# Performance work log

Measured on AMD Instinct MI355X. Metric: run time of the kernel, lower is better.

The kernel has to match this reference:

```python
import jax, jax.numpy as jnp
import numpy as np

N_NODES = 100000   # nodes per node type
N_EDGES = 800000   # edges per edge type
F_IN = 128         # lazy (-1,-1) input feature dim, chosen == hidden
HID = 128          # hidden_channels
OUT = 1            # out_channels
N_LAYERS = 2
B = 256            # batch_size (num graphs)
NEG_SLOPE = 0.2    # GATConv default leaky_relu slope


def setup_inputs() -> dict:
    key = jax.random.key(0)
    ks = jax.random.split(key, 16)
    x_i = jax.random.normal(ks[0], (N_NODES, F_IN), jnp.float32)
    x_j = jax.random.normal(ks[1], (N_NODES, F_IN), jnp.float32)
    ei_ii = jax.random.randint(ks[2], (2, N_EDGES), 0, N_NODES, jnp.int32)
    ei_jj = jax.random.randint(ks[3], (2, N_EDGES), 0, N_NODES, jnp.int32)
    ei_ij = jax.random.randint(ks[4], (2, N_EDGES), 0, N_NODES, jnp.int32)
    ei_ji = jax.random.randint(ks[5], (2, N_EDGES), 0, N_NODES, jnp.int32)
    batch_i = jnp.sort(jax.random.randint(ks[6], (N_NODES,), 0, B, jnp.int32))
    batch_j = jnp.sort(jax.random.randint(ks[7], (N_NODES,), 0, B, jnp.int32))
    s = 1.0 / np.sqrt(HID)
    Ws = jax.random.normal(ks[8], (N_LAYERS, 4, F_IN, HID), jnp.float32) * s
    Wd = jax.random.normal(ks[9], (N_LAYERS, 4, F_IN, HID), jnp.float32) * s
    att_s = jax.random.normal(ks[10], (N_LAYERS, 4, HID), jnp.float32) * s
    att_d = jax.random.normal(ks[11], (N_LAYERS, 4, HID), jnp.float32) * s
    bias = jnp.zeros((N_LAYERS, 4, HID), jnp.float32)
    lin_w = jax.random.normal(ks[12], (HID, OUT), jnp.float32) * s
    lin_b = jnp.zeros((OUT,), jnp.float32)
    return dict(x_i=x_i, x_j=x_j, ei_ii=ei_ii, ei_jj=ei_jj, ei_ij=ei_ij,
                ei_ji=ei_ji, batch_i=batch_i, batch_j=batch_j, Ws=Ws, Wd=Wd,
                att_s=att_s, att_d=att_d, bias=bias, lin_w=lin_w, lin_b=lin_b)


def gat_conv(x_src, x_dst, edge, W_s, W_d, a_s, a_d, b):
    """Single-head GATConv: gather -> edge attention -> segment softmax -> scatter."""
    src, dst = edge[0], edge[1]
    n_dst = x_dst.shape[0]
    hs = x_src @ W_s                      # [Ns, C]
    hd = x_dst @ W_d                      # [Nd, C]
    e = jax.nn.leaky_relu((hs * a_s).sum(-1)[src] + (hd * a_d).sum(-1)[dst],
                          NEG_SLOPE)      # [E]
    m = jax.ops.segment_max(e, dst, num_segments=n_dst)
    m = jnp.where(jnp.isfinite(m), m, 0.0)  # empty segments -> 0
    p = jnp.exp(e - m[dst])
    denom = jax.ops.segment_sum(p, dst, num_segments=n_dst)
    alpha = p / jnp.maximum(denom[dst], 1e-16)
    out = jax.ops.segment_sum(alpha[:, None] * hs[src], dst, num_segments=n_dst)
    return out + b


def mean_pool(x, batch, size):
    s = jax.ops.segment_sum(x, batch, num_segments=size)
    cnt = jax.ops.segment_sum(jnp.ones((x.shape[0],), x.dtype), batch,
                              num_segments=size)
    return s / jnp.maximum(cnt, 1.0)[:, None]


def reference(x_i, x_j, ei_ii, ei_jj, ei_ij, ei_ji, batch_i, batch_j,
              Ws, Wd, att_s, att_d, bias, lin_w, lin_b):
    xi, xj = x_i, x_j
    for l in range(N_LAYERS):
        # edge-type order: 0=inner_i, 1=inner_j, 2=outer_ij, 3=outer_ji
        out_i = (gat_conv(xi, xi, ei_ii, Ws[l, 0], Wd[l, 0], att_s[l, 0], att_d[l, 0], bias[l, 0])
                 + gat_conv(xj, xi, ei_ji, Ws[l, 3], Wd[l, 3], att_s[l, 3], att_d[l, 3], bias[l, 3]))
        out_j = (gat_conv(xj, xj, ei_jj, Ws[l, 1], Wd[l, 1], att_s[l, 1], att_d[l, 1], bias[l, 1])
                 + gat_conv(xi, xj, ei_ij, Ws[l, 2], Wd[l, 2], att_s[l, 2], att_d[l, 2], bias[l, 2]))
        xi, xj = jnp.tanh(out_i), jnp.tanh(out_j)
    p_i = mean_pool(xi, batch_i, B)       # [B, HID]
    p_j = mean_pool(xj, batch_j, B)       # [B, HID]
    x = 0.5 * (p_i + p_j)                 # mean over the stacked pair
    return jax.nn.sigmoid(x @ lin_w + lin_b)
```

## Files before the change

kernel.cpp:

```cpp
#include <hip/hip_runtime.h>


#define NEG_SLOPE 0.2f

typedef __attribute__((ext_vector_type(8))) short short8v;
typedef __attribute__((ext_vector_type(4))) float float4v;

__device__ __forceinline__ unsigned short f2bf(float f) {
  unsigned u = __float_as_uint(f);
  unsigned r = (u + 0x7FFFu + ((u >> 16) & 1u)) >> 16;
  return (unsigned short)r;
}
__device__ __forceinline__ unsigned pack2(float a, float b) {
  return (unsigned)f2bf(a) | ((unsigned)f2bf(b) << 16);
}
__device__ __forceinline__ float bflo(unsigned u) {
  return __uint_as_float(u << 16);
}
__device__ __forceinline__ float bfhi(unsigned u) {
  return __uint_as_float(u & 0xFFFF0000u);
}
__device__ __forceinline__ float rl_f(float x, int lane) {
  return __int_as_float(__builtin_amdgcn_readlane(__float_as_int(x), lane));
}
__device__ __forceinline__ int rl_i(int x, int lane) {
  return __builtin_amdgcn_readlane(x, lane);
}

__global__ __launch_bounds__(256) void w_to_bf16t(const float* __restrict__ W,
                                                  unsigned short* __restrict__ Wt) {
  __shared__ float buf[64][129];
  int b = blockIdx.x, t = threadIdx.x;
  const float* w = W + (size_t)b * 16384;
  unsigned short* o = Wt + (size_t)b * 16384;
  for (int h = 0; h < 2; ++h) {
    for (int i = 0; i < 32; ++i) {
      int idx = i * 256 + t;
      buf[idx >> 7][idx & 127] = w[(size_t)(h * 64 + (idx >> 7)) * 128 + (idx & 127)];
    }
    __syncthreads();
    for (int i = 0; i < 32; ++i) {
      int idx = i * 256 + t;
      o[(size_t)(idx >> 6) * 128 + h * 64 + (idx & 63)] = f2bf(buf[idx & 63][idx >> 6]);
    }
    __syncthreads();
  }
}

__global__ void precompute_wa(const float* __restrict__ W,
                              const float* __restrict__ att,
                              float* __restrict__ out) {
  int idx = blockIdx.x;
  int f = threadIdx.x;
  const float* w = W + (size_t)idx * 128 * 128 + (size_t)f * 128;
  const float* a = att + idx * 128;
  float s = 0.f;
  #pragma unroll 8
  for (int h = 0; h < 128; ++h) s += w[h] * a[h];
  out[idx * 128 + f] = s;
}

template <int XBF16>
__global__ __launch_bounds__(256) void gemm_dual(
    const void* __restrict__ Xv,
    const unsigned short* __restrict__ Wt1, const float* __restrict__ att1,
    unsigned short* __restrict__ Hb1, float* __restrict__ as1,
    const unsigned short* __restrict__ Wt2, const float* __restrict__ att2,
    unsigned short* __restrict__ Hb2, float* __restrict__ as2,
    const float* __restrict__ vdA, const float* __restrict__ vdB,
    float* __restrict__ adA, float* __restrict__ adB, int M) {
  __shared__ unsigned short Xt[64][136];
  __shared__ unsigned short Wt[128][136];
  const int t = threadIdx.x;
  const int row0 = blockIdx.x * 64;

  {
    int r = t >> 2;
    int cq = (t & 3) * 32;
    int gr = row0 + r;
    if (gr >= M) gr = M - 1;
    if (XBF16) {
      const unsigned short* Xb = (const unsigned short*)Xv;
      const uint4* src = (const uint4*)(Xb + (size_t)gr * 128 + cq);
      #pragma unroll
      for (int i = 0; i < 4; ++i) *(uint4*)&Xt[r][cq + i * 8] = src[i];
    } else {
      const float* Xf = (const float*)Xv;
      const float4* src = (const float4*)(Xf + (size_t)gr * 128 + cq);
      #pragma unroll
      for (int i = 0; i < 8; ++i) {
        float4 v = src[i];
        uint2 u;
        u.x = pack2(v.x, v.y);
        u.y = pack2(v.z, v.w);
        *(uint2*)&Xt[r][cq + i * 4] = u;
      }
    }
  }
  {
    int n = t >> 1;
    int kh = (t & 1) * 64;
    const uint4* src = (const uint4*)(Wt1 + (size_t)n * 128 + kh);
    #pragma unroll
    for (int i = 0; i < 8; ++i) *(uint4*)&Wt[n][kh + i * 8] = src[i];
  }
  __syncthreads();

  if (t < 128) {
    int r = t & 63;
    const float* vd = (t < 64) ? vdA : vdB;
    float* adout = (t < 64) ? adA : adB;
    float sum = 0.f;
    #pragma unroll 4
    for (int k8 = 0; k8 < 16; ++k8) {
      uint4 u = *(const uint4*)&Xt[r][k8 * 8];
      const float* v = vd + k8 * 8;
      sum = fmaf(bflo(u.x), v[0], sum);
      sum = fmaf(bfhi(u.x), v[1], sum);
      sum = fmaf(bflo(u.y), v[2], sum);
      sum = fmaf(bfhi(u.y), v[3], sum);
      sum = fmaf(bflo(u.z), v[4], sum);
      sum = fmaf(bfhi(u.z), v[5], sum);
      sum = fmaf(bflo(u.w), v[6], sum);
      sum = fmaf(bfhi(u.w), v[7], sum);
    }
    int gr = row0 + r;
    if (gr < M) adout[gr] = sum;
  }

  const int lane = t & 63;
  const int wv = t >> 6;
  const int m = lane & 15;
  const int g = lane >> 4;
  const int ws = wv * 16;

  for (int ww = 0; ww < 2; ++ww) {
    if (ww == 1) {
      __syncthreads();
      int n = t >> 1;
      int kh = (t & 1) * 64;
      const uint4* src = (const uint4*)(Wt2 + (size_t)n * 128 + kh);
      #pragma unroll
      for (int i = 0; i < 8; ++i) *(uint4*)&Wt[n][kh + i * 8] = src[i];
      __syncthreads();
    }
    const float* att = ww ? att2 : att1;
    unsigned short* Hb = ww ? Hb2 : Hb1;
    float* as_ = ww ? as2 : as1;

    float4v acc[8];
    float4v z = {0.f, 0.f, 0.f, 0.f};
    #pragma unroll
    for (int nt = 0; nt < 8; ++nt) acc[nt] = z;

    #pragma unroll
    for (int ks = 0; ks < 4; ++ks) {
      short8v a = *(const short8v*)&Xt[ws + m][ks * 32 + g * 8];
      #pragma unroll
      for (int nt = 0; nt < 8; ++nt) {
        short8v b = *(const short8v*)&Wt[nt * 16 + m][ks * 32 + g * 8];
        acc[nt] = __builtin_amdgcn_mfma_f32_16x16x32_bf16(a, b, acc[nt], 0, 0, 0);
      }
    }

    {
      float attv[8];
      #pragma unroll
      for (int nt = 0; nt < 8; ++nt) attv[nt] = att[nt * 16 + m];
      #pragma unroll
      for (int r = 0; r < 4; ++r) {
        float s = 0.f;
        #pragma unroll
        for (int nt = 0; nt < 8; ++nt) s = fmaf(acc[nt][r], attv[nt], s);
        #pragma unroll
        for (int off = 1; off < 16; off <<= 1) s += __shfl_xor(s, off);
        if (m == 0) {
          int grow = row0 + ws + g * 4 + r;
          if (grow < M) as_[grow] = s;
        }
      }
    }

    #pragma unroll
    for (int nt = 0; nt < 8; ++nt) {
      #pragma unroll
      for (int r = 0; r < 4; ++r) {
        float v = acc[nt][r];
        float vn = __shfl_xor(v, 1);
        if ((m & 1) == 0) {
          int grow = row0 + ws + g * 4 + r;
          if (grow < M) {
            *(unsigned*)(Hb + (size_t)grow * 128 + nt * 16 + m) = pack2(v, vn);
          }
        }
      }
    }
  }
}

__global__ void hist4(const int* __restrict__ e0, const int* __restrict__ e1,
                      const int* __restrict__ e2, const int* __restrict__ e3,
                      int E, int* __restrict__ deg, int N) {
  int i = blockIdx.x * 256 + threadIdx.x;
  if (i >= E) return;
  int t = blockIdx.y;
  const int* ei = (t == 0) ? e0 : (t == 1) ? e1 : (t == 2) ? e2 : e3;
  atomicAdd(&deg[t * N + ei[E + i]], 1);
}

__global__ __launch_bounds__(1024) void scan4(const int* __restrict__ deg,
                                              int* __restrict__ rowptr, int N) {
  __shared__ int sums[1024];
  int t = threadIdx.x;
  int ty = blockIdx.x;
  const int* d = deg + (size_t)ty * N;
  int* rp = rowptr + (size_t)ty * (N + 1);
  int chunk = (N + 1023) / 1024;
  int lo = t * chunk;
  int hi = lo + chunk; if (hi > N) hi = N; if (lo > N) lo = N;
  int s = 0;
  for (int i = lo; i < hi; ++i) s += d[i];
  sums[t] = s;
  __syncthreads();
  for (int off = 1; off < 1024; off <<= 1) {
    int add = (t >= off) ? sums[t - off] : 0;
    __syncthreads();
    sums[t] += add;
    __syncthreads();
  }
  int run = (t == 0) ? 0 : sums[t - 1];
  for (int i = lo; i < hi; ++i) {
    rp[i] = run;
    run += d[i];
  }
  if (t == 1023) rp[N] = sums[1023];
}

__global__ void fill4(const int* __restrict__ e0, const int* __restrict__ e1,
                      const int* __restrict__ e2, const int* __restrict__ e3,
                      int E, const int* __restrict__ rowptr,
                      int* __restrict__ fill, int* __restrict__ csrc, int N) {
  int i = blockIdx.x * 256 + threadIdx.x;
  if (i >= E) return;
  int t = blockIdx.y;
  const int* ei = (t == 0) ? e0 : (t == 1) ? e1 : (t == 2) ? e2 : e3;
  int d = ei[E + i];
  int s = ei[i];
  int pos = rowptr[(size_t)t * (N + 1) + d] + atomicAdd(&fill[t * N + d], 1);
  csrc[(size_t)t * E + pos] = s;
}

struct PairArgs {
  const int* rA; const int* sA; const unsigned short* hA;
  const float* asA; const float* adA;
  const int* rB; const int* sB; const unsigned short* hB;
  const float* asB; const float* adB;
  const float* biasA; const float* biasB;
};

__device__ __forceinline__ void agg_pair(const PairArgs& P, int n, int lane,
                                         float2& outA, float2& outB) {
  int begA = P.rA[n], endA = P.rA[n + 1];
  int begB = P.rB[n], endB = P.rB[n + 1];
  float adA = P.adA[n], adB = P.adB[n];
  float lsA = 0.f, lsB = 0.f;
  float2 aA = make_float2(0.f, 0.f), aB = make_float2(0.f, 0.f);
  int cA = begA, cB = begB;
  while (cA < endA || cB < endB) {
    int kA = cA + lane, kB = cB + lane;
    bool vA = kA < endA;
    bool vB = kB < endB;
    int sA = vA ? P.sA[kA] : 0;
    int sB = vB ? P.sB[kB] : 0;
    float eA = vA ? (P.asA[sA] + adA) : 0.f;
    float eB = vB ? (P.asB[sB] + adB) : 0.f;
    eA = eA > 0.f ? eA : NEG_SLOPE * eA;
    eB = eB > 0.f ? eB : NEG_SLOPE * eB;
    float pA = vA ? __expf(eA) : 0.f;
    float pB = vB ? __expf(eB) : 0.f;
    int cntA = endA - cA; cntA = cntA < 0 ? 0 : (cntA > 64 ? 64 : cntA);
    int cntB = endB - cB; cntB = cntB < 0 ? 0 : (cntB > 64 ? 64 : cntB);
    int cnt = cntA > cntB ? cntA : cntB;
    for (int base = 0; base < cnt; base += 8) {
      float qa0 = rl_f(pA, base + 0), qa1 = rl_f(pA, base + 1);
      float qa2 = rl_f(pA, base + 2), qa3 = rl_f(pA, base + 3);
      float qa4 = rl_f(pA, base + 4), qa5 = rl_f(pA, base + 5);
      float qa6 = rl_f(pA, base + 6), qa7 = rl_f(pA, base + 7);
      float qb0 = rl_f(pB, base + 0), qb1 = rl_f(pB, base + 1);
      float qb2 = rl_f(pB, base + 2), qb3 = rl_f(pB, base + 3);
      float qb4 = rl_f(pB, base + 4), qb5 = rl_f(pB, base + 5);
      float qb6 = rl_f(pB, base + 6), qb7 = rl_f(pB, base + 7);
      int ta0 = rl_i(sA, base + 0), ta1 = rl_i(sA, base + 1);
      int ta2 = rl_i(sA, base + 2), ta3 = rl_i(sA, base + 3);
      int ta4 = rl_i(sA, base + 4), ta5 = rl_i(sA, base + 5);
      int ta6 = rl_i(sA, base + 6), ta7 = rl_i(sA, base + 7);
      int tb0 = rl_i(sB, base + 0), tb1 = rl_i(sB, base + 1);
      int tb2 = rl_i(sB, base + 2), tb3 = rl_i(sB, base + 3);
      int tb4 = rl_i(sB, base + 4), tb5 = rl_i(sB, base + 5);
      int tb6 = rl_i(sB, base + 6), tb7 = rl_i(sB, base + 7);
      unsigned ua0 = *(const unsigned*)(P.hA + (size_t)ta0 * 128 + lane * 2);
      unsigned ua1 = *(const unsigned*)(P.hA + (size_t)ta1 * 128 + lane * 2);
      unsigned ua2 = *(const unsigned*)(P.hA + (size_t)ta2 * 128 + lane * 2);
      unsigned ua3 = *(const unsigned*)(P.hA + (size_t)ta3 * 128 + lane * 2);
      unsigned ua4 = *(const unsigned*)(P.hA + (size_t)ta4 * 128 + lane * 2);
      unsigned ua5 = *(const unsigned*)(P.hA + (size_t)ta5 * 128 + lane * 2);
      unsigned ua6 = *(const unsigned*)(P.hA + (size_t)ta6 * 128 + lane * 2);
      unsigned ua7 = *(const unsigned*)(P.hA + (size_t)ta7 * 128 + lane * 2);
      unsigned ub0 = *(const unsigned*)(P.hB + (size_t)tb0 * 128 + lane * 2);
      unsigned ub1 = *(const unsigned*)(P.hB + (size_t)tb1 * 128 + lane * 2);
      unsigned ub2 = *(const unsigned*)(P.hB + (size_t)tb2 * 128 + lane * 2);
      unsigned ub3 = *(const unsigned*)(P.hB + (size_t)tb3 * 128 + lane * 2);
      unsigned ub4 = *(const unsigned*)(P.hB + (size_t)tb4 * 128 + lane * 2);
      unsigned ub5 = *(const unsigned*)(P.hB + (size_t)tb5 * 128 + lane * 2);
      unsigned ub6 = *(const unsigned*)(P.hB + (size_t)tb6 * 128 + lane * 2);
      unsigned ub7 = *(const unsigned*)(P.hB + (size_t)tb7 * 128 + lane * 2);
      lsA += ((qa0 + qa1) + (qa2 + qa3)) + ((qa4 + qa5) + (qa6 + qa7));
      lsB += ((qb0 + qb1) + (qb2 + qb3)) + ((qb4 + qb5) + (qb6 + qb7));
      aA.x = fmaf(qa0, bflo(ua0), aA.x); aA.y = fmaf(qa0, bfhi(ua0), aA.y);
      aA.x = fmaf(qa1, bflo(ua1), aA.x); aA.y = fmaf(qa1, bfhi(ua1), aA.y);
      aA.x = fmaf(qa2, bflo(ua2), aA.x); aA.y = fmaf(qa2, bfhi(ua2), aA.y);
      aA.x = fmaf(qa3, bflo(ua3), aA.x); aA.y = fmaf(qa3, bfhi(ua3), aA.y);
      aA.x = fmaf(qa4, bflo(ua4), aA.x); aA.y = fmaf(qa4, bfhi(ua4), aA.y);
      aA.x = fmaf(qa5, bflo(ua5), aA.x); aA.y = fmaf(qa5, bfhi(ua5), aA.y);
      aA.x = fmaf(qa6, bflo(ua6), aA.x); aA.y = fmaf(qa6, bfhi(ua6), aA.y);
      aA.x = fmaf(qa7, bflo(ua7), aA.x); aA.y = fmaf(qa7, bfhi(ua7), aA.y);
      aB.x = fmaf(qb0, bflo(ub0), aB.x); aB.y = fmaf(qb0, bfhi(ub0), aB.y);
      aB.x = fmaf(qb1, bflo(ub1), aB.x); aB.y = fmaf(qb1, bfhi(ub1), aB.y);
      aB.x = fmaf(qb2, bflo(ub2), aB.x); aB.y = fmaf(qb2, bfhi(ub2), aB.y);
      aB.x = fmaf(qb3, bflo(ub3), aB.x); aB.y = fmaf(qb3, bfhi(ub3), aB.y);
      aB.x = fmaf(qb4, bflo(ub4), aB.x); aB.y = fmaf(qb4, bfhi(ub4), aB.y);
      aB.x = fmaf(qb5, bflo(ub5), aB.x); aB.y = fmaf(qb5, bfhi(ub5), aB.y);
      aB.x = fmaf(qb6, bflo(ub6), aB.x); aB.y = fmaf(qb6, bfhi(ub6), aB.y);
      aB.x = fmaf(qb7, bflo(ub7), aB.x); aB.y = fmaf(qb7, bfhi(ub7), aB.y);
    }
    cA += 64;
    cB += 64;
  }
  float invA = 1.f / fmaxf(lsA, 1e-16f);
  float invB = 1.f / fmaxf(lsB, 1e-16f);
  outA = make_float2(aA.x * invA, aA.y * invA);
  outB = make_float2(aB.x * invB, aB.y * invB);
}

__global__ __launch_bounds__(256) void agg_store2(
    PairArgs P0, unsigned short* __restrict__ out0,
    PairArgs P1, unsigned short* __restrict__ out1, int N) {
  int wave = (blockIdx.x * 256 + threadIdx.x) >> 6;
  int lane = threadIdx.x & 63;
  if (wave >= N) return;
  const PairArgs& P = blockIdx.y ? P1 : P0;
  unsigned short* out = blockIdx.y ? out1 : out0;
  float2 a, b;
  agg_pair(P, wave, lane, a, b);
  float2 b1 = *(const float2*)(P.biasA + lane * 2);
  float2 b2 = *(const float2*)(P.biasB + lane * 2);
  float vx = tanhf(a.x + b.x + b1.x + b2.x);
  float vy = tanhf(a.y + b.y + b1.y + b2.y);
  *(unsigned*)(out + (size_t)wave * 128 + lane * 2) = pack2(vx, vy);
}

__global__ __launch_bounds__(256) void agg_pool2(
    PairArgs P0, const int* __restrict__ batch0, float* __restrict__ pool0,
    PairArgs P1, const int* __restrict__ batch1, float* __restrict__ pool1,
    int N) {
  int wave = (blockIdx.x * 256 + threadIdx.x) >> 6;
  int lane = threadIdx.x & 63;
  if (wave >= N) return;
  const PairArgs& P = blockIdx.y ? P1 : P0;
  const int* batch = blockIdx.y ? batch1 : batch0;
  float* pool = blockIdx.y ? pool1 : pool0;
  float2 a, b;
  agg_pair(P, wave, lane, a, b);
  float2 b1 = *(const float2*)(P.biasA + lane * 2);
  float2 b2 = *(const float2*)(P.biasB + lane * 2);
  float vx = tanhf(a.x + b.x + b1.x + b2.x);
  float vy = tanhf(a.y + b.y + b1.y + b2.y);
  int bb = batch[wave];
  float* p = pool + (size_t)bb * 128 + lane * 2;
  unsafeAtomicAdd(p, vx);
  unsafeAtomicAdd(p + 1, vy);
}

__device__ __forceinline__ int lower_bound_i(const int* __restrict__ a, int n,
                                             int v) {
  int lo = 0, hi = n;
  while (lo < hi) {
    int mid = (lo + hi) >> 1;
    if (a[mid] < v) lo = mid + 1; else hi = mid;
  }
  return lo;
}

__global__ void final_k(const float* __restrict__ pool_i,
                        const int* __restrict__ batch_i,
                        const float* __restrict__ pool_j,
                        const int* __restrict__ batch_j, int N,
                        const float* __restrict__ lin_w,
                        const float* __restrict__ lin_b,
                        float* __restrict__ out) {
  int b = threadIdx.x;
  float ci = (float)(lower_bound_i(batch_i, N, b + 1) -
                     lower_bound_i(batch_i, N, b));
  float cj = (float)(lower_bound_i(batch_j, N, b + 1) -
                     lower_bound_i(batch_j, N, b));
  ci = fmaxf(ci, 1.f);
  cj = fmaxf(cj, 1.f);
  float acc = 0.f;
  #pragma unroll 4
  for (int f = 0; f < 128; ++f) {
    float x = 0.5f * (pool_i[(size_t)b * 128 + f] / ci +
                      pool_j[(size_t)b * 128 + f] / cj);
    acc += x * lin_w[f];
  }
  acc += lin_b[0];
  out[b] = 1.f / (1.f + __expf(-acc));
}

extern "C" void kernel_launch(void* const* d_in, const int* in_sizes, int n_in,
                              void* d_out, int out_size, void* d_ws,
                              size_t ws_size, hipStream_t stream) {
  const float* x_i = (const float*)d_in[0];
  const float* x_j = (const float*)d_in[1];
  const int* ei_arr[4] = {(const int*)d_in[2], (const int*)d_in[3],
                          (const int*)d_in[4], (const int*)d_in[5]};
  const int* batch_i = (const int*)d_in[6];
  const int* batch_j = (const int*)d_in[7];
  const float* Ws = (const float*)d_in[8];
  const float* Wd = (const float*)d_in[9];
  const float* att_s = (const float*)d_in[10];
  const float* att_d = (const float*)d_in[11];
  const float* bias = (const float*)d_in[12];
  const float* lin_w = (const float*)d_in[13];
  const float* lin_b = (const float*)d_in[14];
  float* out = (float*)d_out;

  const int N = in_sizes[0] / 128;
  const int E = in_sizes[2] / 2;
  const size_t NF = (size_t)N * 128;

  char* w = (char*)d_ws;
  auto alloc = [&](size_t bytes) {
    char* p = w;
    w += (bytes + 255) & ~(size_t)255;
    return p;
  };
  unsigned short* bufA_i = (unsigned short*)alloc(NF * 2);
  unsigned short* bufA_j = (unsigned short*)alloc(NF * 2);
  unsigned short* hsb[4];
  for (int c = 0; c < 4; ++c) hsb[c] = (unsigned short*)alloc(NF * 2);
  int* csrc = (int*)alloc((size_t)4 * E * 4);
  int* rowptr = (int*)alloc((size_t)4 * (N + 1) * 4);
  int* deg = (int*)alloc((size_t)4 * N * 4);
  int* fillc = (int*)alloc((size_t)4 * N * 4);
  float* asb[4];
  for (int c = 0; c < 4; ++c) asb[c] = (float*)alloc((size_t)N * 4);
  float* adb[4];
  for (int c = 0; c < 4; ++c) adb[c] = (float*)alloc((size_t)N * 4);
  float* wdad = (float*)alloc(8 * 128 * 4);
  unsigned short* Wst = (unsigned short*)alloc(8 * 16384 * 2);
  float* pool = (float*)alloc(2 * 256 * 128 * 4);
  float* pool_i = pool;
  float* pool_j = pool + 256 * 128;

  w_to_bf16t<<<8, 256, 0, stream>>>(Ws, Wst);
  precompute_wa<<<8, 128, 0, stream>>>(Wd, att_d, wdad);

  hipMemsetAsync(deg, 0, (size_t)4 * N * 4, stream);
  hipMemsetAsync(fillc, 0, (size_t)4 * N * 4, stream);
  dim3 egrid((E + 255) / 256, 4);
  hist4<<<egrid, 256, 0, stream>>>(ei_arr[0], ei_arr[1], ei_arr[2], ei_arr[3],
                                   E, deg, N);
  scan4<<<4, 1024, 0, stream>>>(deg, rowptr, N);
  fill4<<<egrid, 256, 0, stream>>>(ei_arr[0], ei_arr[1], ei_arr[2], ei_arr[3],
                                   E, rowptr, fillc, csrc, N);

  hipMemsetAsync(pool, 0, 2 * 256 * 128 * 4, stream);

  const int gemm_blocks = (N + 63) / 64;
  const int nodew_blocks = (N + 3) / 4;

  for (int l = 0; l < 2; ++l) {
    const void* cur_i = (l == 0) ? (const void*)x_i : (const void*)bufA_i;
    const void* cur_j = (l == 0) ? (const void*)x_j : (const void*)bufA_j;
    const size_t L = (size_t)l * 4;

    if (l == 0) {
      gemm_dual<0><<<gemm_blocks, 256, 0, stream>>>(
          cur_i, Wst + (L + 0) * 16384, att_s + (L + 0) * 128, hsb[0], asb[0],
          Wst + (L + 2) * 16384, att_s + (L + 2) * 128, hsb[2], asb[2],
          wdad + (L + 0) * 128, wdad + (L + 3) * 128, adb[0], adb[3], N);
      gemm_dual<0><<<gemm_blocks, 256, 0, stream>>>(
          cur_j, Wst + (L + 1) * 16384, att_s + (L + 1) * 128, hsb[1], asb[1],
          Wst + (L + 3) * 16384, att_s + (L + 3) * 128, hsb[3], asb[3],
          wdad + (L + 1) * 128, wdad + (L + 2) * 128, adb[1], adb[2], N);
    } else {
      gemm_dual<1><<<gemm_blocks, 256, 0, stream>>>(
          cur_i, Wst + (L + 0) * 16384, att_s + (L + 0) * 128, hsb[0], asb[0],
          Wst + (L + 2) * 16384, att_s + (L + 2) * 128, hsb[2], asb[2],
          wdad + (L + 0) * 128, wdad + (L + 3) * 128, adb[0], adb[3], N);
      gemm_dual<1><<<gemm_blocks, 256, 0, stream>>>(
          cur_j, Wst + (L + 1) * 16384, att_s + (L + 1) * 128, hsb[1], asb[1],
          Wst + (L + 3) * 16384, att_s + (L + 3) * 128, hsb[3], asb[3],
          wdad + (L + 1) * 128, wdad + (L + 2) * 128, adb[1], adb[2], N);
    }

    PairArgs P0 = {rowptr + (size_t)0 * (N + 1), csrc + (size_t)0 * E, hsb[0],
                   asb[0], adb[0],
                   rowptr + (size_t)3 * (N + 1), csrc + (size_t)3 * E, hsb[3],
                   asb[3], adb[3],
                   bias + (L + 0) * 128, bias + (L + 3) * 128};
    PairArgs P1 = {rowptr + (size_t)1 * (N + 1), csrc + (size_t)1 * E, hsb[1],
                   asb[1], adb[1],
                   rowptr + (size_t)2 * (N + 1), csrc + (size_t)2 * E, hsb[2],
                   asb[2], adb[2],
                   bias + (L + 1) * 128, bias + (L + 2) * 128};

    dim3 agrid(nodew_blocks, 2);
    if (l == 0) {
      agg_store2<<<agrid, 256, 0, stream>>>(P0, bufA_i, P1, bufA_j, N);
    } else {
      agg_pool2<<<agrid, 256, 0, stream>>>(P0, batch_i, pool_i, P1, batch_j,
                                           pool_j, N);
    }
  }

  final_k<<<1, 256, 0, stream>>>(pool_i, batch_i, pool_j, batch_j, N, lin_w,
                                 lin_b, out);
}
```

Baseline: 1.109 ms.

## Store projected features as fp8, merge dual GEMM launches, grid-stride edge kernels

The per-edge-type projected source features are now stored as packed fp8 instead of bf16 and unpacked with the hardware fp8-to-f32 conversion in the aggregation gather, halving the bytes fetched per gathered neighbour row. The two per-layer GEMM launches are merged into one 2D grid that picks its inputs from blockIdx.y. The histogram and CSR-fill kernels switch to a fixed 512-block grid-stride loop. fp8 storage adds noticeable quantization error to the messages and may break accuracy tolerance.

Result: faster. 1.036 ms, median of 2 (-6.6%).

```diff
diff --git a/kernel.cpp b/kernel.cpp
--- a/kernel.cpp
+++ b/kernel.cpp
@@ -5,6 +5,7 @@
 
 typedef __attribute__((ext_vector_type(8))) short short8v;
 typedef __attribute__((ext_vector_type(4))) float float4v;
+typedef __attribute__((ext_vector_type(2))) float float2v;
 
 __device__ __forceinline__ unsigned short f2bf(float f) {
   unsigned u = __float_as_uint(f);
@@ -60,19 +61,25 @@
   out[idx * 128 + f] = s;
 }
 
+struct GemmArgs {
+  const unsigned short* Wt1; const float* att1;
+  unsigned char* Hb1; float* as1;
+  const unsigned short* Wt2; const float* att2;
+  unsigned char* Hb2; float* as2;
+  const float* vdA; const float* vdB;
+  float* adA; float* adB;
+};
+
 template <int XBF16>
-__global__ __launch_bounds__(256) void gemm_dual(
-    const void* __restrict__ Xv,
-    const unsigned short* __restrict__ Wt1, const float* __restrict__ att1,
-    unsigned short* __restrict__ Hb1, float* __restrict__ as1,
-    const unsigned short* __restrict__ Wt2, const float* __restrict__ att2,
-    unsigned short* __restrict__ Hb2, float* __restrict__ as2,
-    const float* __restrict__ vdA, const float* __restrict__ vdB,
-    float* __restrict__ adA, float* __restrict__ adB, int M) {
+__global__ __launch_bounds__(256) void gemm_dual2(
+    const void* __restrict__ X0, const void* __restrict__ X1,
+    GemmArgs Ga, GemmArgs Gb, int M) {
   __shared__ unsigned short Xt[64][136];
   __shared__ unsigned short Wt[128][136];
   const int t = threadIdx.x;
   const int row0 = blockIdx.x * 64;
+  const void* Xv = blockIdx.y ? X1 : X0;
+  const GemmArgs& G = blockIdx.y ? Gb : Ga;
 
   {
     int r = t >> 2;
@@ -100,7 +107,7 @@
   {
     int n = t >> 1;
     int kh = (t & 1) * 64;
-    const uint4* src = (const uint4*)(Wt1 + (size_t)n * 128 + kh);
+    const uint4* src = (const uint4*)(G.Wt1 + (size_t)n * 128 + kh);
     #pragma unroll
     for (int i = 0; i < 8; ++i) *(uint4*)&Wt[n][kh + i * 8] = src[i];
   }
@@ -108,8 +115,8 @@
 
   if (t < 128) {
     int r = t & 63;
-    const float* vd = (t < 64) ? vdA : vdB;
-    float* adout = (t < 64) ? adA : adB;
+    const float* vd = (t < 64) ? G.vdA : G.vdB;
+    float* adout = (t < 64) ? G.adA : G.adB;
     float sum = 0.f;
     #pragma unroll 4
     for (int k8 = 0; k8 < 16; ++k8) {
@@ -139,14 +146,14 @@
       __syncthreads();
       int n = t >> 1;
       int kh = (t & 1) * 64;
-      const uint4* src = (const uint4*)(Wt2 + (size_t)n * 128 + kh);
+      const uint4* src = (const uint4*)(G.Wt2 + (size_t)n * 128 + kh);
       #pragma unroll
       for (int i = 0; i < 8; ++i) *(uint4*)&Wt[n][kh + i * 8] = src[i];
       __syncthreads();
     }
-    const float* att = ww ? att2 : att1;
-    unsigned short* Hb = ww ? Hb2 : Hb1;
-    float* as_ = ww ? as2 : as1;
+    const float* att = ww ? G.att2 : G.att1;
+    unsigned char* Hb = ww ? G.Hb2 : G.Hb1;
+    float* as_ = ww ? G.as2 : G.as1;
 
     float4v acc[8];
     float4v z = {0.f, 0.f, 0.f, 0.f};
@@ -190,7 +197,9 @@
         if ((m & 1) == 0) {
           int grow = row0 + ws + g * 4 + r;
           if (grow < M) {
-            *(unsigned*)(Hb + (size_t)grow * 128 + nt * 16 + m) = pack2(v, vn);
+            int pk = __builtin_amdgcn_cvt_pk_fp8_f32(v, vn, 0, false);
+            *(unsigned short*)(Hb + (size_t)grow * 128 + nt * 16 + m) =
+                (unsigned short)(pk & 0xFFFF);
           }
         }
       }
@@ -201,11 +210,11 @@
 __global__ void hist4(const int* __restrict__ e0, const int* __restrict__ e1,
                       const int* __restrict__ e2, const int* __restrict__ e3,
                       int E, int* __restrict__ deg, int N) {
-  int i = blockIdx.x * 256 + threadIdx.x;
-  if (i >= E) return;
   int t = blockIdx.y;
   const int* ei = (t == 0) ? e0 : (t == 1) ? e1 : (t == 2) ? e2 : e3;
-  atomicAdd(&deg[t * N + ei[E + i]], 1);
+  int stride = gridDim.x * 256;
+  for (int i = blockIdx.x * 256 + threadIdx.x; i < E; i += stride)
+    atomicAdd(&deg[t * N + ei[E + i]], 1);
 }
 
 __global__ __launch_bounds__(1024) void scan4(const int* __restrict__ deg,
@@ -240,23 +249,28 @@
                       const int* __restrict__ e2, const int* __restrict__ e3,
                       int E, const int* __restrict__ rowptr,
                       int* __restrict__ fill, int* __restrict__ csrc, int N) {
-  int i = blockIdx.x * 256 + threadIdx.x;
-  if (i >= E) return;
   int t = blockIdx.y;
   const int* ei = (t == 0) ? e0 : (t == 1) ? e1 : (t == 2) ? e2 : e3;
-  int d = ei[E + i];
-  int s = ei[i];
-  int pos = rowptr[(size_t)t * (N + 1) + d] + atomicAdd(&fill[t * N + d], 1);
-  csrc[(size_t)t * E + pos] = s;
+  int stride = gridDim.x * 256;
+  for (int i = blockIdx.x * 256 + threadIdx.x; i < E; i += stride) {
+    int d = ei[E + i];
+    int s = ei[i];
+    int pos = rowptr[(size_t)t * (N + 1) + d] + atomicAdd(&fill[t * N + d], 1);
+    csrc[(size_t)t * E + pos] = s;
+  }
 }
 
 struct PairArgs {
-  const int* rA; const int* sA; const unsigned short* hA;
+  const int* rA; const int* sA; const unsigned char* hA;
   const float* asA; const float* adA;
-  const int* rB; const int* sB; const unsigned short* hB;
+  const int* rB; const int* sB; const unsigned char* hB;
   const float* asB; const float* adB;
   const float* biasA; const float* biasB;
 };
+
+#define GATH(P_h, idx, dst) {                                           \
+  unsigned short uu = *(const unsigned short*)((P_h) + (size_t)(idx) * 128 + lane * 2); \
+  dst = __builtin_amdgcn_cvt_pk_f32_fp8((int)uu, false); }
 
 __device__ __forceinline__ void agg_pair(const PairArgs& P, int n, int lane,
                                          float2& outA, float2& outB) {
@@ -298,40 +312,34 @@
       int tb2 = rl_i(sB, base + 2), tb3 = rl_i(sB, base + 3);
       int tb4 = rl_i(sB, base + 4), tb5 = rl_i(sB, base + 5);
       int tb6 = rl_i(sB, base + 6), tb7 = rl_i(sB, base + 7);
-      unsigned ua0 = *(const unsigned*)(P.hA + (size_t)ta0 * 128 + lane * 2);
-      unsigned ua1 = *(const unsigned*)(P.hA + (size_t)ta1 * 128 + lane * 2);
-      unsigned ua2 = *(const unsigned*)(P.hA + (size_t)ta2 * 128 + lane * 2);
-      unsigned ua3 = *(const unsigned*)(P.hA + (size_t)ta3 * 128 + lane * 2);
-      unsigned ua4 = *(const unsigned*)(P.hA + (size_t)ta4 * 128 + lane * 2);
-      unsigned ua5 = *(const unsigned*)(P.hA + (size_t)ta5 * 128 + lane * 2);
-      unsigned ua6 = *(const unsigned*)(P.hA + (size_t)ta6 * 128 + lane * 2);
-      unsigned ua7 = *(const unsigned*)(P.hA + (size_t)ta7 * 128 + lane * 2);
-      unsigned ub0 = *(const unsigned*)(P.hB + (size_t)tb0 * 128 + lane * 2);
-      unsigned ub1 = *(const unsigned*)(P.hB + (size_t)tb1 * 128 + lane * 2);
-      unsigned ub2 = *(const unsigned*)(P.hB + (size_t)tb2 * 128 + lane * 2);
-      unsigned ub3 = *(const unsigned*)(P.hB + (size_t)tb3 * 128 + lane * 2);
-      unsigned ub4 = *(const unsigned*)(P.hB + (size_t)tb4 * 128 + lane * 2);
-      unsigned ub5 = *(const unsigned*)(P.hB + (size_t)tb5 * 128 + lane * 2);
-      unsigned ub6 = *(const unsigned*)(P.hB + (size_t)tb6 * 128 + lane * 2);
-      unsigned ub7 = *(const unsigned*)(P.hB + (size_t)tb7 * 128 + lane * 2);
+      float2v ha0, ha1, ha2, ha3, ha4, ha5, ha6, ha7;
+      float2v hb0, hb1, hb2, hb3, hb4, hb5, hb6, hb7;
+      GATH(P.hA, ta0, ha0) GATH(P.hA, ta1, ha1)
+      GATH(P.hA, ta2, ha2) GATH(P.hA, ta3, ha3)
+      GATH(P.hA, ta4, ha4) GATH(P.hA, ta5, ha5)
+      GATH(P.hA, ta6, ha6) GATH(P.hA, ta7, ha7)
+      GATH(P.hB, tb0, hb0) GATH(P.hB, tb1, hb1)
+      GATH(P.hB, tb2, hb2) GATH(P.hB, tb3, hb3)
+      GATH(P.hB, tb4, hb4) GATH(P.hB, tb5, hb5)
+      GATH(P.hB, tb6, hb6) GATH(P.hB, tb7, hb7)
       lsA += ((qa0 + qa1) + (qa2 + qa3)) + ((qa4 + qa5) + (qa6 + qa7));
       lsB += ((qb0 + qb1) + (qb2 + qb3)) + ((qb4 + qb5) + (qb6 + qb7));
-      aA.x = fmaf(qa0, bflo(ua0), aA.x); aA.y = fmaf(qa0, bfhi(ua0), aA.y);
-      aA.x = fmaf(qa1, bflo(ua1), aA.x); aA.y = fmaf(qa1, bfhi(ua1), aA.y);
-      aA.x = fmaf(qa2, bflo(ua2), aA.x); aA.y = fmaf(qa2, bfhi(ua2), aA.y);
-      aA.x = fmaf(qa3, bflo(ua3), aA.x); aA.y = fmaf(qa3, bfhi(ua3), aA.y);
-      aA.x = fmaf(qa4, bflo(ua4), aA.x); aA.y = fmaf(qa4, bfhi(ua4), aA.y);
-      aA.x = fmaf(qa5, bflo(ua5), aA.x); aA.y = fmaf(qa5, bfhi(ua5), aA.y);
-      aA.x = fmaf(qa6, bflo(ua6), aA.x); aA.y = fmaf(qa6, bfhi(ua6), aA.y);
-      aA.x = fmaf(qa7, bflo(ua7), aA.x); aA.y = fmaf(qa7, bfhi(ua7), aA.y);
-      aB.x = fmaf(qb0, bflo(ub0), aB.x); aB.y = fmaf(qb0, bfhi(ub0), aB.y);
-      aB.x = fmaf(qb1, bflo(ub1), aB.x); aB.y = fmaf(qb1, bfhi(ub1), aB.y);
-      aB.x = fmaf(qb2, bflo(ub2), aB.x); aB.y = fmaf(qb2, bfhi(ub2), aB.y);
-      aB.x = fmaf(qb3, bflo(ub3), aB.x); aB.y = fmaf(qb3, bfhi(ub3), aB.y);
-      aB.x = fmaf(qb4, bflo(ub4), aB.x); aB.y = fmaf(qb4, bfhi(ub4), aB.y);
-      aB.x = fmaf(qb5, bflo(ub5), aB.x); aB.y = fmaf(qb5, bfhi(ub5), aB.y);
-      aB.x = fmaf(qb6, bflo(ub6), aB.x); aB.y = fmaf(qb6, bfhi(ub6), aB.y);
-      aB.x = fmaf(qb7, bflo(ub7), aB.x); aB.y = fmaf(qb7, bfhi(ub7), aB.y);
+      aA.x = fmaf(qa0, ha0[0], aA.x); aA.y = fmaf(qa0, ha0[1], aA.y);
+      aA.x = fmaf(qa1, ha1[0], aA.x); aA.y = fmaf(qa1, ha1[1], aA.y);
+      aA.x = fmaf(qa2, ha2[0], aA.x); aA.y = fmaf(qa2, ha2[1], aA.y);
+      aA.x = fmaf(qa3, ha3[0], aA.x); aA.y = fmaf(qa3, ha3[1], aA.y);
+      aA.x = fmaf(qa4, ha4[0], aA.x); aA.y = fmaf(qa4, ha4[1], aA.y);
+      aA.x = fmaf(qa5, ha5[0], aA.x); aA.y = fmaf(qa5, ha5[1], aA.y);
+      aA.x = fmaf(qa6, ha6[0], aA.x); aA.y = fmaf(qa6, ha6[1], aA.y);
+      aA.x = fmaf(qa7, ha7[0], aA.x); aA.y = fmaf(qa7, ha7[1], aA.y);
+      aB.x = fmaf(qb0, hb0[0], aB.x); aB.y = fmaf(qb0, hb0[1], aB.y);
+      aB.x = fmaf(qb1, hb1[0], aB.x); aB.y = fmaf(qb1, hb1[1], aB.y);
+      aB.x = fmaf(qb2, hb2[0], aB.x); aB.y = fmaf(qb2, hb2[1], aB.y);
+      aB.x = fmaf(qb3, hb3[0], aB.x); aB.y = fmaf(qb3, hb3[1], aB.y);
+      aB.x = fmaf(qb4, hb4[0], aB.x); aB.y = fmaf(qb4, hb4[1], aB.y);
+      aB.x = fmaf(qb5, hb5[0], aB.x); aB.y = fmaf(qb5, hb5[1], aB.y);
+      aB.x = fmaf(qb6, hb6[0], aB.x); aB.y = fmaf(qb6, hb6[1], aB.y);
+      aB.x = fmaf(qb7, hb7[0], aB.x); aB.y = fmaf(qb7, hb7[1], aB.y);
     }
     cA += 64;
     cB += 64;
@@ -446,8 +454,8 @@
   };
   unsigned short* bufA_i = (unsigned short*)alloc(NF * 2);
   unsigned short* bufA_j = (unsigned short*)alloc(NF * 2);
-  unsigned short* hsb[4];
-  for (int c = 0; c < 4; ++c) hsb[c] = (unsigned short*)alloc(NF * 2);
+  unsigned char* hsb[4];
+  for (int c = 0; c < 4; ++c) hsb[c] = (unsigned char*)alloc(NF);
   int* csrc = (int*)alloc((size_t)4 * E * 4);
   int* rowptr = (int*)alloc((size_t)4 * (N + 1) * 4);
   int* deg = (int*)alloc((size_t)4 * N * 4);
@@ -467,7 +475,7 @@
 
   hipMemsetAsync(deg, 0, (size_t)4 * N * 4, stream);
   hipMemsetAsync(fillc, 0, (size_t)4 * N * 4, stream);
-  dim3 egrid((E + 255) / 256, 4);
+  dim3 egrid(512, 4);
   hist4<<<egrid, 256, 0, stream>>>(ei_arr[0], ei_arr[1], ei_arr[2], ei_arr[3],
                                    E, deg, N);
   scan4<<<4, 1024, 0, stream>>>(deg, rowptr, N);
@@ -484,24 +492,17 @@
     const void* cur_j = (l == 0) ? (const void*)x_j : (const void*)bufA_j;
     const size_t L = (size_t)l * 4;
 
+    GemmArgs Ga = {Wst + (L + 0) * 16384, att_s + (L + 0) * 128, hsb[0], asb[0],
+                   Wst + (L + 2) * 16384, att_s + (L + 2) * 128, hsb[2], asb[2],
+                   wdad + (L + 0) * 128, wdad + (L + 3) * 128, adb[0], adb[3]};
+    GemmArgs Gb = {Wst + (L + 1) * 16384, att_s + (L + 1) * 128, hsb[1], asb[1],
+                   Wst + (L + 3) * 16384, att_s + (L + 3) * 128, hsb[3], asb[3],
+                   wdad + (L + 1) * 128, wdad + (L + 2) * 128, adb[1], adb[2]};
+    dim3 ggrid(gemm_blocks, 2);
     if (l == 0) {
-      gemm_dual<0><<<gemm_blocks, 256, 0, stream>>>(
-          cur_i, Wst + (L + 0) * 16384, att_s + (L + 0) * 128, hsb[0], asb[0],
-          Wst + (L + 2) * 16384, att_s + (L + 2) * 128, hsb[2], asb[2],
-          wdad + (L + 0) * 128, wdad + (L + 3) * 128, adb[0], adb[3], N);
-      gemm_dual<0><<<gemm_blocks, 256, 0, stream>>>(
-          cur_j, Wst + (L + 1) * 16384, att_s + (L + 1) * 128, hsb[1], asb[1],
-          Wst + (L + 3) * 16384, att_s + (L + 3) * 128, hsb[3], asb[3],
-          wdad + (L + 1) * 128, wdad + (L + 2) * 128, adb[1], adb[2], N);
+      gemm_dual2<0><<<ggrid, 256, 0, stream>>>(cur_i, cur_j, Ga, Gb, N);
     } else {
-      gemm_dual<1><<<gemm_blocks, 256, 0, stream>>>(
-          cur_i, Wst + (L + 0) * 16384, att_s + (L + 0) * 128, hsb[0], asb[0],
-          Wst + (L + 2) * 16384, att_s + (L + 2) * 128, hsb[2], asb[2],
-          wdad + (L + 0) * 128, wdad + (L + 3) * 128, adb[0], adb[3], N);
-      gemm_dual<1><<<gemm_blocks, 256, 0, stream>>>(
-          cur_j, Wst + (L + 1) * 16384, att_s + (L + 1) * 128, hsb[1], asb[1],
-          Wst + (L + 3) * 16384, att_s + (L + 3) * 128, hsb[3], asb[3],
-          wdad + (L + 1) * 128, wdad + (L + 2) * 128, adb[1], adb[2], N);
+      gemm_dual2<1><<<ggrid, 256, 0, stream>>>(cur_i, cur_j, Ga, Gb, N);
     }
 
     PairArgs P0 = {rowptr + (size_t)0 * (N + 1), csrc + (size_t)0 * E, hsb[0],
```
